# Performance work log

Hardware: AMD Instinct MI355X
Metric: run time of the kernel (lower is better)

## Reference

```python
import jax, jax.numpy as jnp
import numpy as np

D = 256
FF = 1024
NH = 8
BZ, TL = 8, 1024
L, Hs, Ws = 1, 64, 64


def _linear(x, w, b):
    # torch nn.Linear convention: w is [out, in]
    return x @ w.T + b


def _ln(x, g, b, eps=1e-5):
    m = x.mean(-1, keepdims=True)
    v = ((x - m) ** 2).mean(-1, keepdims=True)
    return (x - m) / jnp.sqrt(v + eps) * g + b


def setup_inputs() -> dict:
    key = jax.random.key(0)
    ks = jax.random.split(key, 16)
    s = 0.02
    inp = {
        "tgt": jax.random.normal(ks[0], (BZ, TL, D), jnp.float32),
        "reference_points": jax.random.uniform(ks[1], (BZ, TL, 2), jnp.float32),
        "srcs": jax.random.normal(ks[2], (BZ, L, D, Hs, Ws), jnp.float32),
        "posemb_2d": jax.random.normal(ks[3], (BZ, TL, D), jnp.float32),
        # self-attn (nn.MultiheadAttention) params
        "in_proj_w": jax.random.normal(ks[4], (3 * D, D), jnp.float32) * s,
        "in_proj_b": jnp.zeros((3 * D,), jnp.float32),
        "out_proj_w": jax.random.normal(ks[5], (D, D), jnp.float32) * s,
        "out_proj_b": jnp.zeros((D,), jnp.float32),
        # hand-rolled cross-attn linears (q, k, v, out)
        "lin_q_w": jax.random.normal(ks[6], (D, D), jnp.float32) * s,
        "lin_q_b": jnp.zeros((D,), jnp.float32),
        "lin_k_w": jax.random.normal(ks[7], (D, D), jnp.float32) * s,
        "lin_k_b": jnp.zeros((D,), jnp.float32),
        "lin_v_w": jax.random.normal(ks[8], (D, D), jnp.float32) * s,
        "lin_v_b": jnp.zeros((D,), jnp.float32),
        "lin_o_w": jax.random.normal(ks[9], (D, D), jnp.float32) * s,
        "lin_o_b": jnp.zeros((D,), jnp.float32),
        # layer norms
        "norm1_g": jnp.ones((D,), jnp.float32),
        "norm1_b": jnp.zeros((D,), jnp.float32),
        "norm2_g": jnp.ones((D,), jnp.float32),
        "norm2_b": jnp.zeros((D,), jnp.float32),
        # FFN
        "ffn_w1": jax.random.normal(ks[10], (FF, D), jnp.float32) * s,
        "ffn_b1": jnp.zeros((FF,), jnp.float32),
        "ffn_w2": jax.random.normal(ks[11], (D, FF), jnp.float32) * s,
        "ffn_b2": jnp.zeros((D,), jnp.float32),
        "ffn_norm_g": jnp.ones((D,), jnp.float32),
        "ffn_norm_b": jnp.zeros((D,), jnp.float32),
    }
    return inp


def reference(tgt, reference_points, srcs, posemb_2d,
              in_proj_w, in_proj_b, out_proj_w, out_proj_b,
              lin_q_w, lin_q_b, lin_k_w, lin_k_b, lin_v_w, lin_v_b,
              lin_o_w, lin_o_b,
              norm1_g, norm1_b, norm2_g, norm2_b,
              ffn_w1, ffn_b1, ffn_w2, ffn_b2, ffn_norm_g, ffn_norm_b):
    bz, tl, c = tgt.shape
    nh = NH
    dh = c // nh
    scale = dh ** -0.5

    # ---- self-attention (nn.MultiheadAttention math) ----
    qk = tgt + posemb_2d  # q = k = with_pos_embed(tgt, posemb_2d_)
    wq, wk, wv = in_proj_w[:c], in_proj_w[c:2 * c], in_proj_w[2 * c:]
    bq, bk, bv = in_proj_b[:c], in_proj_b[c:2 * c], in_proj_b[2 * c:]
    qp = _linear(qk, wq, bq).reshape(bz, tl, nh, dh)
    kp = _linear(qk, wk, bk).reshape(bz, tl, nh, dh)
    vp = _linear(tgt, wv, bv).reshape(bz, tl, nh, dh)
    att = jax.nn.softmax(jnp.einsum('bqhd,bkhd->bhqk', qp * scale, kp), axis=-1)
    sa = jnp.einsum('bhqk,bkhd->bqhd', att, vp).reshape(bz, tl, c)
    sa = _linear(sa, out_proj_w, out_proj_b)
    tgt = _ln(tgt + sa, norm2_g, norm2_b)

    # ---- hand-rolled cross attention ----
    bz_, l, c_, h, w = srcs.shape
    s = jnp.transpose(srcs.reshape(bz_ * l, c_, h, w), (0, 2, 3, 1)).reshape(bz_ * l, h * w, c_)
    query = _linear(tgt, lin_q_w, lin_q_b)          # [bz, tl, c]
    key = _linear(s, lin_k_w, lin_k_b)              # [bz*l, hw, c]
    value = _linear(s, lin_v_w, lin_v_b)
    affinity = jax.nn.softmax(jnp.einsum('bqc,bkc->bqk', query, key), axis=-1)  # no 1/sqrt(d) scale, faithful
    tgt2 = _linear(jnp.einsum('bqk,bkc->bqc', affinity, value), lin_o_w, lin_o_b)
    tgt = _ln(tgt + tgt2, norm1_g, norm1_b)

    # ---- FFN ----
    src2 = _linear(jax.nn.relu(_linear(tgt, ffn_w1, ffn_b1)), ffn_w2, ffn_b2)
    tgt = _ln(tgt + src2, ffn_norm_g, ffn_norm_b)
    return tgt
```

## Files before the change

kernel.cpp:

```cpp
#include <hip/hip_runtime.h>
#include <hip/hip_bf16.h>
#include <math.h>

typedef __attribute__((ext_vector_type(8))) __bf16 bf16x8;
typedef __attribute__((ext_vector_type(4))) __bf16 bf16x4;
typedef __attribute__((ext_vector_type(2))) __bf16 bf16x2;
typedef __attribute__((ext_vector_type(4))) float  f32x4;

#define MFMA16(a,b,c) __builtin_amdgcn_mfma_f32_16x16x32_bf16((a),(b),(c),0,0,0)

__device__ __forceinline__ unsigned pack2bf(float a, float b){
  bf16x2 t; t[0] = (__bf16)a; t[1] = (__bf16)b;
  return __builtin_bit_cast(unsigned, t);
}

template<int BM, bool RELU, int OUTMODE>
__global__ __launch_bounds__(256) void gemm_bt(
    const float* __restrict__ A, const float* __restrict__ W,
    const float* __restrict__ bias, void* __restrict__ Cv,
    int M, int N, int K, int ldc, int coff, float oscale)
{
  constexpr int MT = BM/32;
  __shared__ __align__(16) __bf16 As[BM][40];
  __shared__ __align__(16) __bf16 Bs[64][40];

  const int tid  = threadIdx.x;
  const int wid  = tid >> 6;
  const int lane = tid & 63;
  const int wr   = wid >> 1;
  const int wc   = wid & 1;
  const int lq   = lane & 15;
  const int lk8  = (lane >> 4) << 3;
  const int rb   = (lane >> 4) << 2;

  const int m0 = blockIdx.x * BM;
  const int n0 = blockIdx.y * 64;

  const int scg = (tid & 7) << 2;
  const int sr  = tid >> 3;

  f32x4 acc[MT][2];
  #pragma unroll
  for (int i=0;i<MT;i++)
    #pragma unroll
    for (int j=0;j<2;j++) acc[i][j] = f32x4{0.f,0.f,0.f,0.f};

  for (int k0=0; k0<K; k0+=32){
    __syncthreads();
    #pragma unroll
    for (int i=0;i<MT;i++){
      const int row = sr + i*32;
      const float4 a4 = *(const float4*)&A[(size_t)(m0+row)*K + k0 + scg];
      bf16x4 h; h[0]=(__bf16)a4.x; h[1]=(__bf16)a4.y; h[2]=(__bf16)a4.z; h[3]=(__bf16)a4.w;
      *(bf16x4*)&As[row][scg] = h;
    }
    #pragma unroll
    for (int i=0;i<2;i++){
      const int row = sr + i*32;
      const float4 a4 = *(const float4*)&W[(size_t)(n0+row)*K + k0 + scg];
      bf16x4 h; h[0]=(__bf16)a4.x; h[1]=(__bf16)a4.y; h[2]=(__bf16)a4.z; h[3]=(__bf16)a4.w;
      *(bf16x4*)&Bs[row][scg] = h;
    }
    __syncthreads();
    bf16x8 af[MT], bfr[2];
    #pragma unroll
    for (int i=0;i<MT;i++) af[i]  = *(const bf16x8*)&As[wr*(BM/2) + i*16 + lq][lk8];
    #pragma unroll
    for (int j=0;j<2;j++)  bfr[j] = *(const bf16x8*)&Bs[wc*32 + j*16 + lq][lk8];
    #pragma unroll
    for (int i=0;i<MT;i++)
      #pragma unroll
      for (int j=0;j<2;j++)
        acc[i][j] = MFMA16(af[i], bfr[j], acc[i][j]);
  }

  #pragma unroll
  for (int i=0;i<MT;i++)
    #pragma unroll
    for (int j=0;j<2;j++){
      const int coln = n0 + wc*32 + j*16 + lq;
      const float bv = bias ? bias[coln] : 0.f;
      if (OUTMODE == 2){
        const int rowm0 = m0 + wr*(BM/2) + i*16 + rb;
        bf16x4 hv;
        #pragma unroll
        for (int r=0;r<4;r++){
          float vv = (acc[i][j][r] + bv) * oscale;
          if (RELU) vv = fmaxf(vv, 0.f);
          hv[r] = (__bf16)vv;
        }
        *(bf16x4*)&((__bf16*)Cv)[((size_t)((rowm0>>10)*256) + coln)*1024 + (rowm0&1023)] = hv;
      } else {
        #pragma unroll
        for (int r=0;r<4;r++){
          const int rowm = m0 + wr*(BM/2) + i*16 + rb + r;
          float vv = (acc[i][j][r] + bv) * oscale;
          if (RELU) vv = fmaxf(vv, 0.f);
          const size_t idx = (size_t)rowm*ldc + coff + coln;
          if (OUTMODE == 1) ((__bf16*)Cv)[idx] = (__bf16)vv;
          else              ((float*)Cv)[idx]  = vv;
        }
      }
    }
}

template<bool TRANSOUT>
__global__ __launch_bounds__(256) void gemm_srcs(
    const float* __restrict__ S, const float* __restrict__ W,
    const float* __restrict__ bias, __bf16* __restrict__ C)
{
  __shared__ __align__(16) __bf16 As[128][40];
  __shared__ __align__(16) __bf16 Bs[64][40];

  const int tid  = threadIdx.x;
  const int wid  = tid >> 6;
  const int lane = tid & 63;
  const int wr   = wid >> 1;
  const int wc   = wid & 1;
  const int lq   = lane & 15;
  const int lk8  = (lane >> 4) << 3;
  const int rb   = (lane >> 4) << 2;

  const int m0 = blockIdx.x * 128;
  const int n0 = blockIdx.y * 64;
  const int bb = m0 >> 12;
  const int p0 = m0 & 4095;

  const int cA = tid & 31;
  const int qA = tid >> 5;
  const int scg = (tid & 7) << 2;
  const int sr  = tid >> 3;

  f32x4 acc[4][2];
  #pragma unroll
  for (int i=0;i<4;i++)
    #pragma unroll
    for (int j=0;j<2;j++) acc[i][j] = f32x4{0.f,0.f,0.f,0.f};

  for (int k0=0; k0<256; k0+=32){
    __syncthreads();
    const float* sbase = &S[((size_t)bb*256 + k0 + cA)*4096 + p0];
    #pragma unroll
    for (int ps=0; ps<4; ps++){
      const int p = ps*32 + qA*4;
      const float4 f4 = *(const float4*)(sbase + p);
      As[p+0][cA] = (__bf16)f4.x;
      As[p+1][cA] = (__bf16)f4.y;
      As[p+2][cA] = (__bf16)f4.z;
      As[p+3][cA] = (__bf16)f4.w;
    }
    #pragma unroll
    for (int i=0;i<2;i++){
      const int row = sr + i*32;
      const float4 a4 = *(const float4*)&W[(size_t)(n0+row)*256 + k0 + scg];
      bf16x4 h; h[0]=(__bf16)a4.x; h[1]=(__bf16)a4.y; h[2]=(__bf16)a4.z; h[3]=(__bf16)a4.w;
      *(bf16x4*)&Bs[row][scg] = h;
    }
    __syncthreads();
    bf16x8 af[4], bfr[2];
    #pragma unroll
    for (int i=0;i<4;i++) af[i]  = *(const bf16x8*)&As[wr*64 + i*16 + lq][lk8];
    #pragma unroll
    for (int j=0;j<2;j++) bfr[j] = *(const bf16x8*)&Bs[wc*32 + j*16 + lq][lk8];
    #pragma unroll
    for (int i=0;i<4;i++)
      #pragma unroll
      for (int j=0;j<2;j++)
        acc[i][j] = MFMA16(af[i], bfr[j], acc[i][j]);
  }

  #pragma unroll
  for (int i=0;i<4;i++)
    #pragma unroll
    for (int j=0;j<2;j++){
      const int coln = n0 + wc*32 + j*16 + lq;
      const float bv = bias ? bias[coln] : 0.f;
      if (TRANSOUT){
        bf16x4 hv;
        #pragma unroll
        for (int r=0;r<4;r++) hv[r] = (__bf16)(acc[i][j][r] + bv);
        *(bf16x4*)&C[((size_t)bb*256 + coln)*4096 + p0 + wr*64 + i*16 + rb] = hv;
      } else {
        #pragma unroll
        for (int r=0;r<4;r++){
          const int rowm = m0 + wr*64 + i*16 + rb + r;
          C[(size_t)rowm*256 + coln] = (__bf16)(acc[i][j][r] + bv);
        }
      }
    }
}

__global__ __launch_bounds__(256) void add_vec4(const float* __restrict__ a,
                                                const float* __restrict__ b,
                                                float* __restrict__ o, int n4)
{
  const int i = blockIdx.x*blockDim.x + threadIdx.x;
  if (i < n4){
    const float4 x = ((const float4*)a)[i];
    const float4 y = ((const float4*)b)[i];
    float4 z; z.x=x.x+y.x; z.y=x.y+y.y; z.z=x.z+y.z; z.w=x.w+y.w;
    ((float4*)o)[i] = z;
  }
}

__global__ __launch_bounds__(256) void ln_kernel(const float* __restrict__ res,
                                                 const float* __restrict__ x,
                                                 const float* __restrict__ g,
                                                 const float* __restrict__ beta,
                                                 float* __restrict__ out)
{
  const int row  = blockIdx.x*4 + (threadIdx.x >> 6);
  const int lane = threadIdx.x & 63;
  const int c = lane*4;
  const float4 rv = *(const float4*)&res[(size_t)row*256 + c];
  const float4 xv = *(const float4*)&x[(size_t)row*256 + c];
  float v0=rv.x+xv.x, v1=rv.y+xv.y, v2=rv.z+xv.z, v3=rv.w+xv.w;
  float s = v0+v1+v2+v3;
  #pragma unroll
  for (int off=1; off<64; off<<=1) s += __shfl_xor(s, off);
  const float mean = s * (1.f/256.f);
  const float d0=v0-mean, d1=v1-mean, d2=v2-mean, d3=v3-mean;
  float q = d0*d0 + d1*d1 + d2*d2 + d3*d3;
  #pragma unroll
  for (int off=1; off<64; off<<=1) q += __shfl_xor(q, off);
  const float rstd = rsqrtf(q*(1.f/256.f) + 1e-5f);
  const float4 gv = *(const float4*)&g[c];
  const float4 bv = *(const float4*)&beta[c];
  float4 ov;
  ov.x = d0*rstd*gv.x + bv.x;
  ov.y = d1*rstd*gv.y + bv.y;
  ov.z = d2*rstd*gv.z + bv.z;
  ov.w = d3*rstd*gv.w + bv.w;
  *(float4*)&out[(size_t)row*256 + c] = ov;
}

__global__ __launch_bounds__(256) void flash_self(
    const __bf16* __restrict__ qs, const __bf16* __restrict__ ks,
    const __bf16* __restrict__ vts, float* __restrict__ sa)
{
  const int qt = blockIdx.x;
  const int b  = blockIdx.y >> 3;
  const int h  = blockIdx.y & 7;
  const int tid  = threadIdx.x;
  const int wid  = tid >> 6;
  const int lane = tid & 63;
  const int lq   = lane & 15;
  const int hi   = lane >> 4;
  const int lk8  = hi << 3;
  const int rb   = hi << 2;

  const int qrow = b*1024 + qt*64 + wid*16 + lq;
  const bf16x8 qf = *(const bf16x8*)&qs[(size_t)qrow*256 + h*32 + lk8];

  const __bf16* kb0 = &ks[(size_t)(b*1024 + lq)*256 + h*32 + lk8];
  const __bf16* vb0 = &vts[(size_t)(b*256 + h*32 + lq)*1024 + lk8];

  const f32x4 Z = {0.f, 0.f, 0.f, 0.f};
  float m = -1e30f, l = 0.f;
  f32x4 o0 = Z, o1 = Z;

  for (int it=0; it<16; ++it){
    const int key0 = it*64;
    f32x4 s4[4];
    #pragma unroll
    for (int kt=0;kt<4;kt++){
      const bf16x8 kf = *(const bf16x8*)(kb0 + (size_t)(key0 + kt*16)*256);
      s4[kt] = MFMA16(kf, qf, Z);
    }
    float pm = s4[0][0];
    #pragma unroll
    for (int kt=0;kt<4;kt++)
      #pragma unroll
      for (int r=0;r<4;r++) pm = fmaxf(pm, s4[kt][r]);
    pm = fmaxf(pm, __shfl_xor(pm,16));
    pm = fmaxf(pm, __shfl_xor(pm,32));
    if (!__all(pm <= m + 8.f)){
      const float mn = fmaxf(m, pm);
      const float alpha = __expf(m - mn);
      o0[0]*=alpha; o0[1]*=alpha; o0[2]*=alpha; o0[3]*=alpha;
      o1[0]*=alpha; o1[1]*=alpha; o1[2]*=alpha; o1[3]*=alpha;
      l *= alpha;
      m = mn;
    }
    float p[4][4]; float rs = 0.f;
    #pragma unroll
    for (int kt=0;kt<4;kt++)
      #pragma unroll
      for (int r=0;r<4;r++){ p[kt][r] = __expf(s4[kt][r]-m); rs += p[kt][r]; }
    rs += __shfl_xor(rs,16);
    rs += __shfl_xor(rs,32);
    l += rs;
    unsigned pk0[4], pk1[4];
    #pragma unroll
    for (int kt=0;kt<4;kt++){
      pk0[kt] = pack2bf(p[kt][0], p[kt][1]);
      pk1[kt] = pack2bf(p[kt][2], p[kt][3]);
    }
    const int srcA = ((hi&1)<<5) + lq;
    const int srcB = srcA + 16;
    const bool ksel = hi >= 2;
    bf16x8 pf[2];
    #pragma unroll
    for (int ks2=0; ks2<2; ks2++){
      const unsigned a0 = (unsigned)__shfl((int)pk0[2*ks2],   srcA);
      const unsigned a1 = (unsigned)__shfl((int)pk0[2*ks2+1], srcA);
      const unsigned b0 = (unsigned)__shfl((int)pk1[2*ks2],   srcA);
      const unsigned b1 = (unsigned)__shfl((int)pk1[2*ks2+1], srcA);
      const unsigned c0 = (unsigned)__shfl((int)pk0[2*ks2],   srcB);
      const unsigned c1 = (unsigned)__shfl((int)pk0[2*ks2+1], srcB);
      const unsigned d0 = (unsigned)__shfl((int)pk1[2*ks2],   srcB);
      const unsigned d1 = (unsigned)__shfl((int)pk1[2*ks2+1], srcB);
      union { unsigned u[4]; bf16x8 v; } uu;
      uu.u[0] = ksel ? a1 : a0;
      uu.u[1] = ksel ? b1 : b0;
      uu.u[2] = ksel ? c1 : c0;
      uu.u[3] = ksel ? d1 : d0;
      pf[ks2] = uu.v;
    }
    #pragma unroll
    for (int ks2=0; ks2<2; ks2++){
      const bf16x8 vf0 = *(const bf16x8*)(vb0 + key0 + ks2*32);
      const bf16x8 vf1 = *(const bf16x8*)(vb0 + (size_t)16*1024 + key0 + ks2*32);
      o0 = MFMA16(vf0, pf[ks2], o0);
      o1 = MFMA16(vf1, pf[ks2], o1);
    }
  }
  const float inv = 1.f / l;
  f32x4 w0, w1;
  #pragma unroll
  for (int r=0;r<4;r++){ w0[r] = o0[r]*inv; w1[r] = o1[r]*inv; }
  *(f32x4*)&sa[(size_t)qrow*256 + h*32 + rb]      = w0;
  *(f32x4*)&sa[(size_t)qrow*256 + h*32 + 16 + rb] = w1;
}

__global__ __launch_bounds__(256, 2) void flash_cross(
    const __bf16* __restrict__ qg, const __bf16* __restrict__ kg,
    const __bf16* __restrict__ vtg, float* __restrict__ Opart,
    float* __restrict__ ml)
{
  extern __shared__ __bf16 smem[];
  __bf16* Ks = smem;
  __bf16* Vt = smem + 64*256;

  const int qt = blockIdx.x;
  const int b  = blockIdx.y;
  const int sl = blockIdx.z;
  const int tid  = threadIdx.x;
  const int wid  = tid >> 6;
  const int lane = tid & 63;
  const int lq   = lane & 15;
  const int hi   = lane >> 4;
  const int lk8  = hi << 3;
  const int rb   = hi << 2;
  const int swz  = lq & 7;

  const int qrow = b*1024 + qt*64 + wid*16 + lq;
  bf16x8 qf[8];
  #pragma unroll
  for (int ks=0; ks<8; ks++)
    qf[ks] = *(const bf16x8*)&qg[(size_t)qrow*256 + ks*32 + lk8];

  const f32x4 Z = {0.f, 0.f, 0.f, 0.f};
  float m = -1e30f, l = 0.f;
  f32x4 o[16];
  #pragma unroll
  for (int nf=0; nf<16; nf++) o[nf] = Z;

  const int srow = tid >> 2;
  const int sc4  = tid & 3;

  for (int it=0; it<16; ++it){
    const int key0 = sl*1024 + it*64;
    __syncthreads();
    {
      const __bf16* kb = &kg[(size_t)(b*4096 + key0 + srow)*256];
      #pragma unroll
      for (int j=0;j<8;j++){
        const int ch = sc4 + j*4;
        const bf16x8 vv = *(const bf16x8*)(kb + ch*8);
        *(bf16x8*)&Ks[srow*256 + ((ch ^ (srow&7))<<3)] = vv;
      }
    }
    {
      #pragma unroll
      for (int ps=0; ps<4; ps++){
        const int d = srow + ps*64;
        const __bf16* vb = &vtg[(size_t)(b*256 + d)*4096 + key0];
        #pragma unroll
        for (int s2=0;s2<2;s2++){
          const int ch = sc4 + s2*4;
          const bf16x8 vv = *(const bf16x8*)(vb + ch*8);
          *(bf16x8*)&Vt[d*64 + ((ch ^ (d&7))<<3)] = vv;
        }
      }
    }
    __syncthreads();
    f32x4 s4[4];
    #pragma unroll
    for (int kt=0;kt<4;kt++) s4[kt] = Z;
    #pragma unroll
    for (int ks=0; ks<8; ks++){
      #pragma unroll
      for (int kt=0; kt<4; kt++){
        const bf16x8 kf = *(const bf16x8*)&Ks[(kt*16+lq)*256 + (((ks*4+hi) ^ swz)<<3)];
        s4[kt] = MFMA16(kf, qf[ks], s4[kt]);
      }
    }
    float pm = s4[0][0];
    #pragma unroll
    for (int kt=0;kt<4;kt++)
      #pragma unroll
      for (int r=0;r<4;r++) pm = fmaxf(pm, s4[kt][r]);
    pm = fmaxf(pm, __shfl_xor(pm, 16));
    pm = fmaxf(pm, __shfl_xor(pm, 32));
    if (!__all(pm <= m + 8.f)){
      const float mn = fmaxf(m, pm);
      const float alpha = __expf(m - mn);
      #pragma unroll
      for (int nf=0;nf<16;nf++){
        o[nf][0]*=alpha; o[nf][1]*=alpha; o[nf][2]*=alpha; o[nf][3]*=alpha;
      }
      l *= alpha;
      m = mn;
    }
    float p[4][4];
    float rs = 0.f;
    #pragma unroll
    for (int kt=0;kt<4;kt++)
      #pragma unroll
      for (int r=0;r<4;r++){ p[kt][r] = __expf(s4[kt][r] - m); rs += p[kt][r]; }
    rs += __shfl_xor(rs, 16);
    rs += __shfl_xor(rs, 32);
    l += rs;
    unsigned pk0[4], pk1[4];
    #pragma unroll
    for (int kt=0;kt<4;kt++){
      pk0[kt] = pack2bf(p[kt][0], p[kt][1]);
      pk1[kt] = pack2bf(p[kt][2], p[kt][3]);
    }
    const int srcA = ((hi&1)<<5) + lq;
    const int srcB = srcA + 16;
    const bool ksel = hi >= 2;
    bf16x8 pf[2];
    #pragma unroll
    for (int ks2=0; ks2<2; ks2++){
      const unsigned a0 = (unsigned)__shfl((int)pk0[2*ks2],   srcA);
      const unsigned a1 = (unsigned)__shfl((int)pk0[2*ks2+1], srcA);
      const unsigned b0 = (unsigned)__shfl((int)pk1[2*ks2],   srcA);
      const unsigned b1 = (unsigned)__shfl((int)pk1[2*ks2+1], srcA);
      const unsigned c0 = (unsigned)__shfl((int)pk0[2*ks2],   srcB);
      const unsigned c1 = (unsigned)__shfl((int)pk0[2*ks2+1], srcB);
      const unsigned d0 = (unsigned)__shfl((int)pk1[2*ks2],   srcB);
      const unsigned d1 = (unsigned)__shfl((int)pk1[2*ks2+1], srcB);
      union { unsigned u[4]; bf16x8 v; } uu;
      uu.u[0] = ksel ? a1 : a0;
      uu.u[1] = ksel ? b1 : b0;
      uu.u[2] = ksel ? c1 : c0;
      uu.u[3] = ksel ? d1 : d0;
      pf[ks2] = uu.v;
    }
    #pragma unroll
    for (int nf=0; nf<16; nf++){
      #pragma unroll
      for (int ks2=0; ks2<2; ks2++){
        const bf16x8 af = *(const bf16x8*)&Vt[(nf*16+lq)*64 + (((ks2*4+hi) ^ swz)<<3)];
        o[nf] = MFMA16(af, pf[ks2], o[nf]);
      }
    }
  }
  const int row = b*1024 + qt*64 + wid*16 + lq;
  if (hi == 0){
    ml[(size_t)(sl*8192 + row)*2 + 0] = m;
    ml[(size_t)(sl*8192 + row)*2 + 1] = l;
  }
  #pragma unroll
  for (int nf=0; nf<16; nf++)
    *(f32x4*)&Opart[(size_t)(sl*8192 + row)*256 + nf*16 + rb] = o[nf];
}

__global__ __launch_bounds__(256) void combine_kernel(const float* __restrict__ Opart,
                                                      const float* __restrict__ ml,
                                                      float* __restrict__ out)
{
  const int row = blockIdx.x;
  const int d = threadIdx.x;
  float mm[4], ll[4];
  #pragma unroll
  for (int s=0;s<4;s++){
    mm[s] = ml[(size_t)(s*8192+row)*2 + 0];
    ll[s] = ml[(size_t)(s*8192+row)*2 + 1];
  }
  const float M = fmaxf(fmaxf(mm[0],mm[1]), fmaxf(mm[2],mm[3]));
  float L = 0.f, acc = 0.f;
  #pragma unroll
  for (int s=0;s<4;s++){
    const float e = __expf(mm[s]-M);
    L   += ll[s]*e;
    acc += e * Opart[(size_t)(s*8192+row)*256 + d];
  }
  out[(size_t)row*256 + d] = acc / L;
}

extern "C" void kernel_launch(void* const* d_in, const int* in_sizes, int n_in,
                              void* d_out, int out_size, void* d_ws, size_t ws_size,
                              hipStream_t stream)
{
  (void)in_sizes; (void)n_in; (void)out_size; (void)ws_size;
  const float* tgt        = (const float*)d_in[0];
  const float* srcs       = (const float*)d_in[2];
  const float* posemb     = (const float*)d_in[3];
  const float* in_proj_w  = (const float*)d_in[4];
  const float* in_proj_b  = (const float*)d_in[5];
  const float* out_proj_w = (const float*)d_in[6];
  const float* out_proj_b = (const float*)d_in[7];
  const float* lin_q_w    = (const float*)d_in[8];
  const float* lin_q_b    = (const float*)d_in[9];
  const float* lin_k_w    = (const float*)d_in[10];
  const float* lin_k_b    = (const float*)d_in[11];
  const float* lin_v_w    = (const float*)d_in[12];
  const float* lin_v_b    = (const float*)d_in[13];
  const float* lin_o_w    = (const float*)d_in[14];
  const float* lin_o_b    = (const float*)d_in[15];
  const float* norm1_g    = (const float*)d_in[16];
  const float* norm1_b    = (const float*)d_in[17];
  const float* norm2_g    = (const float*)d_in[18];
  const float* norm2_b    = (const float*)d_in[19];
  const float* ffn_w1     = (const float*)d_in[20];
  const float* ffn_b1     = (const float*)d_in[21];
  const float* ffn_w2     = (const float*)d_in[22];
  const float* ffn_b2     = (const float*)d_in[23];
  const float* ffn_norm_g = (const float*)d_in[24];
  const float* ffn_norm_b = (const float*)d_in[25];
  float* out = (float*)d_out;

  char* w = (char*)d_ws;
  const size_t MB = (size_t)1 << 20;
  float*  tgt1    = (float*)(w + 0);
  float*  qk      = (float*)(w + 8*MB);
  float*  sa      = (float*)(w + 8*MB);
  __bf16* query_b = (__bf16*)(w + 8*MB);
  float*  attn2   = (float*)(w + 8*MB);
  float*  ffn_out = (float*)(w + 8*MB);
  __bf16* q_s     = (__bf16*)(w + 16*MB);
  __bf16* key_b   = (__bf16*)(w + 16*MB);
  float*  t2proj  = (float*)(w + 16*MB);
  __bf16* k_s     = (__bf16*)(w + 20*MB);
  __bf16* v_t     = (__bf16*)(w + 24*MB);
  float*  tgt3    = (float*)(w + 24*MB);
  float*  saproj  = (float*)(w + 28*MB);
  __bf16* val_t   = (__bf16*)(w + 32*MB);
  float*  ffn_h   = (float*)(w + 32*MB);
  float*  Opart   = (float*)(w + 48*MB);
  float*  ml      = (float*)(w + 82*MB);

  const float SCALE = 0.17677669529663687f;

  add_vec4<<<2048,256,0,stream>>>(tgt, posemb, qk, (8*1024*256)/4);
  gemm_bt<64,false,1><<<dim3(128,4),256,0,stream>>>(qk, in_proj_w, in_proj_b,
      q_s, 8192,256,256, 256,0, SCALE);
  gemm_bt<64,false,1><<<dim3(128,4),256,0,stream>>>(qk, in_proj_w + 256*256,
      in_proj_b + 256, k_s, 8192,256,256, 256,0, 1.f);
  gemm_bt<64,false,2><<<dim3(128,4),256,0,stream>>>(tgt, in_proj_w + 512*256,
      in_proj_b + 512, v_t, 8192,256,256, 256,0, 1.f);
  flash_self<<<dim3(16,64),256,0,stream>>>(q_s, k_s, v_t, sa);
  gemm_bt<64,false,0><<<dim3(128,4),256,0,stream>>>(sa, out_proj_w, out_proj_b,
      saproj, 8192,256,256, 256,0, 1.f);
  ln_kernel<<<2048,256,0,stream>>>(tgt, saproj, norm2_g, norm2_b, tgt1);

  gemm_bt<64,false,1><<<dim3(128,4),256,0,stream>>>(tgt1, lin_q_w, lin_q_b,
      query_b, 8192,256,256, 256,0, 1.f);
  gemm_srcs<false><<<dim3(256,4),256,0,stream>>>(srcs, lin_k_w, lin_k_b, key_b);
  gemm_srcs<true ><<<dim3(256,4),256,0,stream>>>(srcs, lin_v_w, lin_v_b, val_t);
  flash_cross<<<dim3(16,8,4),256,65536,stream>>>(query_b, key_b, val_t, Opart, ml);
  combine_kernel<<<8192,256,0,stream>>>(Opart, ml, attn2);
  gemm_bt<64,false,0><<<dim3(128,4),256,0,stream>>>(attn2, lin_o_w, lin_o_b,
      t2proj, 8192,256,256, 256,0, 1.f);
  ln_kernel<<<2048,256,0,stream>>>(tgt1, t2proj, norm1_g, norm1_b, tgt3);

  gemm_bt<128,true,0><<<dim3(64,16),256,0,stream>>>(tgt3, ffn_w1, ffn_b1,
      ffn_h, 8192,1024,256, 1024,0, 1.f);
  gemm_bt<64,false,0><<<dim3(128,4),256,0,stream>>>(ffn_h, ffn_w2, ffn_b2,
      ffn_out, 8192,256,1024, 256,0, 1.f);
  ln_kernel<<<2048,256,0,stream>>>(tgt3, ffn_out, ffn_norm_g, ffn_norm_b, out);
}
```

Measured before the change: 297.1 us.

## Fuse posemb add into QK GEMM and retile cross-attention with bf16 partials

Removes the standalone add kernel by letting the Q/K projection GEMMs load and sum tgt and posemb on the fly. Cross-attention now has each warp handle two 16-row query groups that share every K/V fragment read from LDS. The key split goes from 4 to 8 (512 keys per block, grid 8x8x8), and the swizzle permutation changes. Partial outputs are stored in bf16 instead of fp32, halving combine traffic at some cost in precision, while the extra split raises combine work and register pressure.

```diff
diff --git a/kernel.cpp b/kernel.cpp
--- a/kernel.cpp
+++ b/kernel.cpp
@@ -13,10 +13,12 @@
   bf16x2 t; t[0] = (__bf16)a; t[1] = (__bf16)b;
   return __builtin_bit_cast(unsigned, t);
 }
-
-template<int BM, bool RELU, int OUTMODE>
+__device__ __forceinline__ int perm1(int r){ return ((r<<2)|(r>>1)) & 7; }
+
+template<int BM, bool RELU, int OUTMODE, bool ADD2>
 __global__ __launch_bounds__(256) void gemm_bt(
-    const float* __restrict__ A, const float* __restrict__ W,
+    const float* __restrict__ A, const float* __restrict__ A2,
+    const float* __restrict__ W,
     const float* __restrict__ bias, void* __restrict__ Cv,
     int M, int N, int K, int ldc, int coff, float oscale)
 {
@@ -50,7 +52,11 @@
     #pragma unroll
     for (int i=0;i<MT;i++){
       const int row = sr + i*32;
-      const float4 a4 = *(const float4*)&A[(size_t)(m0+row)*K + k0 + scg];
+      float4 a4 = *(const float4*)&A[(size_t)(m0+row)*K + k0 + scg];
+      if (ADD2){
+        const float4 a42 = *(const float4*)&A2[(size_t)(m0+row)*K + k0 + scg];
+        a4.x+=a42.x; a4.y+=a42.y; a4.z+=a42.z; a4.w+=a42.w;
+      }
       bf16x4 h; h[0]=(__bf16)a4.x; h[1]=(__bf16)a4.y; h[2]=(__bf16)a4.z; h[3]=(__bf16)a4.w;
       *(bf16x4*)&As[row][scg] = h;
     }
@@ -188,19 +194,6 @@
         }
       }
     }
-}
-
-__global__ __launch_bounds__(256) void add_vec4(const float* __restrict__ a,
-                                                const float* __restrict__ b,
-                                                float* __restrict__ o, int n4)
-{
-  const int i = blockIdx.x*blockDim.x + threadIdx.x;
-  if (i < n4){
-    const float4 x = ((const float4*)a)[i];
-    const float4 y = ((const float4*)b)[i];
-    float4 z; z.x=x.x+y.x; z.y=x.y+y.y; z.z=x.z+y.z; z.w=x.w+y.w;
-    ((float4*)o)[i] = z;
-  }
 }
 
 __global__ __launch_bounds__(256) void ln_kernel(const float* __restrict__ res,
@@ -334,8 +327,8 @@
 }
 
 __global__ __launch_bounds__(256, 2) void flash_cross(
-    const __bf16* __restrict__ qg, const __bf16* __restrict__ kg,
-    const __bf16* __restrict__ vtg, float* __restrict__ Opart,
+    const __bf16* __restrict__ qgm, const __bf16* __restrict__ kg,
+    const __bf16* __restrict__ vtg, __bf16* __restrict__ Opart,
     float* __restrict__ ml)
 {
   extern __shared__ __bf16 smem[];
@@ -352,33 +345,38 @@
   const int hi   = lane >> 4;
   const int lk8  = hi << 3;
   const int rb   = hi << 2;
-  const int swz  = lq & 7;
-
-  const int qrow = b*1024 + qt*64 + wid*16 + lq;
-  bf16x8 qf[8];
-  #pragma unroll
-  for (int ks=0; ks<8; ks++)
-    qf[ks] = *(const bf16x8*)&qg[(size_t)qrow*256 + ks*32 + lk8];
+  const int p1l  = perm1(lq & 7);
+
+  const int q0 = b*1024 + qt*128 + wid*32;
+  bf16x8 qf[2][8];
+  #pragma unroll
+  for (int g=0; g<2; g++)
+    #pragma unroll
+    for (int ks=0; ks<8; ks++)
+      qf[g][ks] = *(const bf16x8*)&qgm[(size_t)(q0 + g*16 + lq)*256 + ks*32 + lk8];
 
   const f32x4 Z = {0.f, 0.f, 0.f, 0.f};
-  float m = -1e30f, l = 0.f;
-  f32x4 o[16];
-  #pragma unroll
-  for (int nf=0; nf<16; nf++) o[nf] = Z;
+  float m[2] = {-1e30f, -1e30f};
+  float l[2] = {0.f, 0.f};
+  f32x4 o[2][16];
+  #pragma unroll
+  for (int g=0; g<2; g++)
+    #pragma unroll
+    for (int nf=0; nf<16; nf++) o[g][nf] = Z;
 
   const int srow = tid >> 2;
   const int sc4  = tid & 3;
-
-  for (int it=0; it<16; ++it){
-    const int key0 = sl*1024 + it*64;
+  const int p1s  = perm1(srow & 7);
+
+  for (int it=0; it<8; ++it){
+    const int key0 = sl*512 + it*64;
     __syncthreads();
     {
       const __bf16* kb = &kg[(size_t)(b*4096 + key0 + srow)*256];
       #pragma unroll
       for (int j=0;j<8;j++){
         const int ch = sc4 + j*4;
-        const bf16x8 vv = *(const bf16x8*)(kb + ch*8);
-        *(bf16x8*)&Ks[srow*256 + ((ch ^ (srow&7))<<3)] = vv;
+        *(bf16x8*)&Ks[srow*256 + ((ch ^ p1s)<<3)] = *(const bf16x8*)(kb + ch*8);
       }
     }
     {
@@ -389,114 +387,139 @@
         #pragma unroll
         for (int s2=0;s2<2;s2++){
           const int ch = sc4 + s2*4;
-          const bf16x8 vv = *(const bf16x8*)(vb + ch*8);
-          *(bf16x8*)&Vt[d*64 + ((ch ^ (d&7))<<3)] = vv;
+          *(bf16x8*)&Vt[d*64 + ((ch ^ p1s)<<3)] = *(const bf16x8*)(vb + ch*8);
         }
       }
     }
     __syncthreads();
-    f32x4 s4[4];
-    #pragma unroll
-    for (int kt=0;kt<4;kt++) s4[kt] = Z;
+    f32x4 s4[2][4];
+    #pragma unroll
+    for (int g=0; g<2; g++)
+      #pragma unroll
+      for (int kt=0;kt<4;kt++) s4[g][kt] = Z;
     #pragma unroll
     for (int ks=0; ks<8; ks++){
       #pragma unroll
       for (int kt=0; kt<4; kt++){
-        const bf16x8 kf = *(const bf16x8*)&Ks[(kt*16+lq)*256 + (((ks*4+hi) ^ swz)<<3)];
-        s4[kt] = MFMA16(kf, qf[ks], s4[kt]);
-      }
-    }
-    float pm = s4[0][0];
-    #pragma unroll
-    for (int kt=0;kt<4;kt++)
-      #pragma unroll
-      for (int r=0;r<4;r++) pm = fmaxf(pm, s4[kt][r]);
-    pm = fmaxf(pm, __shfl_xor(pm, 16));
-    pm = fmaxf(pm, __shfl_xor(pm, 32));
-    if (!__all(pm <= m + 8.f)){
-      const float mn = fmaxf(m, pm);
-      const float alpha = __expf(m - mn);
-      #pragma unroll
-      for (int nf=0;nf<16;nf++){
-        o[nf][0]*=alpha; o[nf][1]*=alpha; o[nf][2]*=alpha; o[nf][3]*=alpha;
-      }
-      l *= alpha;
-      m = mn;
-    }
-    float p[4][4];
-    float rs = 0.f;
-    #pragma unroll
-    for (int kt=0;kt<4;kt++)
-      #pragma unroll
-      for (int r=0;r<4;r++){ p[kt][r] = __expf(s4[kt][r] - m); rs += p[kt][r]; }
-    rs += __shfl_xor(rs, 16);
-    rs += __shfl_xor(rs, 32);
-    l += rs;
-    unsigned pk0[4], pk1[4];
-    #pragma unroll
-    for (int kt=0;kt<4;kt++){
-      pk0[kt] = pack2bf(p[kt][0], p[kt][1]);
-      pk1[kt] = pack2bf(p[kt][2], p[kt][3]);
-    }
-    const int srcA = ((hi&1)<<5) + lq;
-    const int srcB = srcA + 16;
-    const bool ksel = hi >= 2;
-    bf16x8 pf[2];
-    #pragma unroll
-    for (int ks2=0; ks2<2; ks2++){
-      const unsigned a0 = (unsigned)__shfl((int)pk0[2*ks2],   srcA);
-      const unsigned a1 = (unsigned)__shfl((int)pk0[2*ks2+1], srcA);
-      const unsigned b0 = (unsigned)__shfl((int)pk1[2*ks2],   srcA);
-      const unsigned b1 = (unsigned)__shfl((int)pk1[2*ks2+1], srcA);
-      const unsigned c0 = (unsigned)__shfl((int)pk0[2*ks2],   srcB);
-      const unsigned c1 = (unsigned)__shfl((int)pk0[2*ks2+1], srcB);
-      const unsigned d0 = (unsigned)__shfl((int)pk1[2*ks2],   srcB);
-      const unsigned d1 = (unsigned)__shfl((int)pk1[2*ks2+1], srcB);
-      union { unsigned u[4]; bf16x8 v; } uu;
-      uu.u[0] = ksel ? a1 : a0;
-      uu.u[1] = ksel ? b1 : b0;
-      uu.u[2] = ksel ? c1 : c0;
-      uu.u[3] = ksel ? d1 : d0;
-      pf[ks2] = uu.v;
+        const bf16x8 kf = *(const bf16x8*)&Ks[(kt*16+lq)*256 + (((ks*4+hi) ^ p1l)<<3)];
+        s4[0][kt] = MFMA16(kf, qf[0][ks], s4[0][kt]);
+        s4[1][kt] = MFMA16(kf, qf[1][ks], s4[1][kt]);
+      }
+    }
+    float pm[2];
+    #pragma unroll
+    for (int g=0; g<2; g++){
+      float v = s4[g][0][0];
+      #pragma unroll
+      for (int kt=0;kt<4;kt++)
+        #pragma unroll
+        for (int r=0;r<4;r++) v = fmaxf(v, s4[g][kt][r]);
+      v = fmaxf(v, __shfl_xor(v, 16));
+      v = fmaxf(v, __shfl_xor(v, 32));
+      pm[g] = v;
+    }
+    const bool need = (pm[0] > m[0] + 8.f) || (pm[1] > m[1] + 8.f);
+    if (__any(need)){
+      #pragma unroll
+      for (int g=0; g<2; g++){
+        const float mn = fmaxf(m[g], pm[g]);
+        const float alpha = __expf(m[g] - mn);
+        #pragma unroll
+        for (int nf=0;nf<16;nf++){
+          o[g][nf][0]*=alpha; o[g][nf][1]*=alpha;
+          o[g][nf][2]*=alpha; o[g][nf][3]*=alpha;
+        }
+        l[g] *= alpha;
+        m[g] = mn;
+      }
+    }
+    bf16x8 pf[2][2];
+    #pragma unroll
+    for (int g=0; g<2; g++){
+      float p[4][4];
+      float rs = 0.f;
+      #pragma unroll
+      for (int kt=0;kt<4;kt++)
+        #pragma unroll
+        for (int r=0;r<4;r++){ p[kt][r] = __expf(s4[g][kt][r] - m[g]); rs += p[kt][r]; }
+      rs += __shfl_xor(rs, 16);
+      rs += __shfl_xor(rs, 32);
+      l[g] += rs;
+      unsigned pk0[4], pk1[4];
+      #pragma unroll
+      for (int kt=0;kt<4;kt++){
+        pk0[kt] = pack2bf(p[kt][0], p[kt][1]);
+        pk1[kt] = pack2bf(p[kt][2], p[kt][3]);
+      }
+      const int srcA = ((hi&1)<<5) + lq;
+      const int srcB = srcA + 16;
+      const bool ksel = hi >= 2;
+      #pragma unroll
+      for (int ks2=0; ks2<2; ks2++){
+        const unsigned a0 = (unsigned)__shfl((int)pk0[2*ks2],   srcA);
+        const unsigned a1 = (unsigned)__shfl((int)pk0[2*ks2+1], srcA);
+        const unsigned b0 = (unsigned)__shfl((int)pk1[2*ks2],   srcA);
+        const unsigned b1 = (unsigned)__shfl((int)pk1[2*ks2+1], srcA);
+        const unsigned c0 = (unsigned)__shfl((int)pk0[2*ks2],   srcB);
+        const unsigned c1 = (unsigned)__shfl((int)pk0[2*ks2+1], srcB);
+        const unsigned d0 = (unsigned)__shfl((int)pk1[2*ks2],   srcB);
+        const unsigned d1 = (unsigned)__shfl((int)pk1[2*ks2+1], srcB);
+        union { unsigned u[4]; bf16x8 v; } uu;
+        uu.u[0] = ksel ? a1 : a0;
+        uu.u[1] = ksel ? b1 : b0;
+        uu.u[2] = ksel ? c1 : c0;
+        uu.u[3] = ksel ? d1 : d0;
+        pf[g][ks2] = uu.v;
+      }
     }
     #pragma unroll
     for (int nf=0; nf<16; nf++){
       #pragma unroll
       for (int ks2=0; ks2<2; ks2++){
-        const bf16x8 af = *(const bf16x8*)&Vt[(nf*16+lq)*64 + (((ks2*4+hi) ^ swz)<<3)];
-        o[nf] = MFMA16(af, pf[ks2], o[nf]);
+        const bf16x8 af = *(const bf16x8*)&Vt[(nf*16+lq)*64 + (((ks2*4+hi) ^ p1l)<<3)];
+        o[0][nf] = MFMA16(af, pf[0][ks2], o[0][nf]);
+        o[1][nf] = MFMA16(af, pf[1][ks2], o[1][nf]);
       }
     }
   }
-  const int row = b*1024 + qt*64 + wid*16 + lq;
-  if (hi == 0){
-    ml[(size_t)(sl*8192 + row)*2 + 0] = m;
-    ml[(size_t)(sl*8192 + row)*2 + 1] = l;
+  #pragma unroll
+  for (int g=0; g<2; g++){
+    const int row = q0 + g*16 + lq;
+    if (hi == 0){
+      ml[(size_t)(sl*8192 + row)*2 + 0] = m[g];
+      ml[(size_t)(sl*8192 + row)*2 + 1] = l[g];
+    }
+    #pragma unroll
+    for (int nf=0; nf<16; nf++){
+      bf16x4 hv;
+      #pragma unroll
+      for (int r=0;r<4;r++) hv[r] = (__bf16)o[g][nf][r];
+      *(bf16x4*)&Opart[(size_t)(sl*8192 + row)*256 + nf*16 + rb] = hv;
+    }
   }
-  #pragma unroll
-  for (int nf=0; nf<16; nf++)
-    *(f32x4*)&Opart[(size_t)(sl*8192 + row)*256 + nf*16 + rb] = o[nf];
-}
-
-__global__ __launch_bounds__(256) void combine_kernel(const float* __restrict__ Opart,
+}
+
+__global__ __launch_bounds__(256) void combine_kernel(const __bf16* __restrict__ Opart,
                                                       const float* __restrict__ ml,
                                                       float* __restrict__ out)
 {
   const int row = blockIdx.x;
   const int d = threadIdx.x;
-  float mm[4], ll[4];
-  #pragma unroll
-  for (int s=0;s<4;s++){
+  float mm[8], ll[8];
+  #pragma unroll
+  for (int s=0;s<8;s++){
     mm[s] = ml[(size_t)(s*8192+row)*2 + 0];
     ll[s] = ml[(size_t)(s*8192+row)*2 + 1];
   }
-  const float M = fmaxf(fmaxf(mm[0],mm[1]), fmaxf(mm[2],mm[3]));
+  float M = mm[0];
+  #pragma unroll
+  for (int s=1;s<8;s++) M = fmaxf(M, mm[s]);
   float L = 0.f, acc = 0.f;
   #pragma unroll
-  for (int s=0;s<4;s++){
+  for (int s=0;s<8;s++){
     const float e = __expf(mm[s]-M);
     L   += ll[s]*e;
-    acc += e * Opart[(size_t)(s*8192+row)*256 + d];
+    acc += e * (float)Opart[(size_t)(s*8192+row)*256 + d];
   }
   out[(size_t)row*256 + d] = acc / L;
 }
@@ -536,7 +559,6 @@
   char* w = (char*)d_ws;
   const size_t MB = (size_t)1 << 20;
   float*  tgt1    = (float*)(w + 0);
-  float*  qk      = (float*)(w + 8*MB);
   float*  sa      = (float*)(w + 8*MB);
   __bf16* query_b = (__bf16*)(w + 8*MB);
   float*  attn2   = (float*)(w + 8*MB);
@@ -550,36 +572,35 @@
   float*  saproj  = (float*)(w + 28*MB);
   __bf16* val_t   = (__bf16*)(w + 32*MB);
   float*  ffn_h   = (float*)(w + 32*MB);
-  float*  Opart   = (float*)(w + 48*MB);
-  float*  ml      = (float*)(w + 82*MB);
+  __bf16* Opart   = (__bf16*)(w + 48*MB);
+  float*  ml      = (float*)(w + 80*MB);
 
   const float SCALE = 0.17677669529663687f;
 
-  add_vec4<<<2048,256,0,stream>>>(tgt, posemb, qk, (8*1024*256)/4);
-  gemm_bt<64,false,1><<<dim3(128,4),256,0,stream>>>(qk, in_proj_w, in_proj_b,
-      q_s, 8192,256,256, 256,0, SCALE);
-  gemm_bt<64,false,1><<<dim3(128,4),256,0,stream>>>(qk, in_proj_w + 256*256,
-      in_proj_b + 256, k_s, 8192,256,256, 256,0, 1.f);
-  gemm_bt<64,false,2><<<dim3(128,4),256,0,stream>>>(tgt, in_proj_w + 512*256,
-      in_proj_b + 512, v_t, 8192,256,256, 256,0, 1.f);
+  gemm_bt<64,false,1,true><<<dim3(128,4),256,0,stream>>>(tgt, posemb,
+      in_proj_w, in_proj_b, q_s, 8192,256,256, 256,0, SCALE);
+  gemm_bt<64,false,1,true><<<dim3(128,4),256,0,stream>>>(tgt, posemb,
+      in_proj_w + 256*256, in_proj_b + 256, k_s, 8192,256,256, 256,0, 1.f);
+  gemm_bt<64,false,2,false><<<dim3(128,4),256,0,stream>>>(tgt, nullptr,
+      in_proj_w + 512*256, in_proj_b + 512, v_t, 8192,256,256, 256,0, 1.f);
   flash_self<<<dim3(16,64),256,0,stream>>>(q_s, k_s, v_t, sa);
-  gemm_bt<64,false,0><<<dim3(128,4),256,0,stream>>>(sa, out_proj_w, out_proj_b,
-      saproj, 8192,256,256, 256,0, 1.f);
+  gemm_bt<64,false,0,false><<<dim3(128,4),256,0,stream>>>(sa, nullptr,
+      out_proj_w, out_proj_b, saproj, 8192,256,256, 256,0, 1.f);
   ln_kernel<<<2048,256,0,stream>>>(tgt, saproj, norm2_g, norm2_b, tgt1);
 
-  gemm_bt<64,false,1><<<dim3(128,4),256,0,stream>>>(tgt1, lin_q_w, lin_q_b,
-      query_b, 8192,256,256, 256,0, 1.f);
+  gemm_bt<64,false,1,false><<<dim3(128,4),256,0,stream>>>(tgt1, nullptr,
+      lin_q_w, lin_q_b, query_b, 8192,256,256, 256,0, 1.f);
   gemm_srcs<false><<<dim3(256,4),256,0,stream>>>(srcs, lin_k_w, lin_k_b, key_b);
   gemm_srcs<true ><<<dim3(256,4),256,0,stream>>>(srcs, lin_v_w, lin_v_b, val_t);
-  flash_cross<<<dim3(16,8,4),256,65536,stream>>>(query_b, key_b, val_t, Opart, ml);
+  flash_cross<<<dim3(8,8,8),256,65536,stream>>>(query_b, key_b, val_t, Opart, ml);
   combine_kernel<<<8192,256,0,stream>>>(Opart, ml, attn2);
-  gemm_bt<64,false,0><<<dim3(128,4),256,0,stream>>>(attn2, lin_o_w, lin_o_b,
-      t2proj, 8192,256,256, 256,0, 1.f);
+  gemm_bt<64,false,0,false><<<dim3(128,4),256,0,stream>>>(attn2, nullptr,
+      lin_o_w, lin_o_b, t2proj, 8192,256,256, 256,0, 1.f);
   ln_kernel<<<2048,256,0,stream>>>(tgt1, t2proj, norm1_g, norm1_b, tgt3);
 
-  gemm_bt<128,true,0><<<dim3(64,16),256,0,stream>>>(tgt3, ffn_w1, ffn_b1,
-      ffn_h, 8192,1024,256, 1024,0, 1.f);
-  gemm_bt<64,false,0><<<dim3(128,4),256,0,stream>>>(ffn_h, ffn_w2, ffn_b2,
-      ffn_out, 8192,256,1024, 256,0, 1.f);
+  gemm_bt<128,true,0,false><<<dim3(64,16),256,0,stream>>>(tgt3, nullptr,
+      ffn_w1, ffn_b1, ffn_h, 8192,1024,256, 1024,0, 1.f);
+  gemm_bt<64,false,0,false><<<dim3(128,4),256,0,stream>>>(ffn_h, nullptr,
+      ffn_w2, ffn_b2, ffn_out, 8192,256,1024, 256,0, 1.f);
   ln_kernel<<<2048,256,0,stream>>>(tgt3, ffn_out, ffn_norm_g, ffn_norm_b, out);
 }
```

After: 348.4 us. +17.2%, slower.
